# Optimization experiments

Hardware: AMD Instinct MI355X
Metric: run time of the kernel (lower is better)

## Reference

```python
import jax, jax.numpy as jnp
import numpy as np

B, S, D, H = 2, 2048, 1024, 16
HD = D // H  # head_dim = 64


def setup_inputs() -> dict:
    key = jax.random.key(0)
    ks = jax.random.split(key, 10)
    std = 1.0 / np.sqrt(D)
    inputs = jax.random.normal(ks[0], (B, S, D), dtype=jnp.float32)
    # stacked per-head projection weights: [H, HD, D] (row-major like nn.Linear)
    Wq = jax.random.uniform(ks[1], (H, HD, D), jnp.float32, -std, std)
    bq = jax.random.uniform(ks[2], (H, HD), jnp.float32, -std, std)
    Wk = jax.random.uniform(ks[3], (H, HD, D), jnp.float32, -std, std)
    bk = jax.random.uniform(ks[4], (H, HD), jnp.float32, -std, std)
    Wv = jax.random.uniform(ks[5], (H, HD, D), jnp.float32, -std, std)
    bv = jax.random.uniform(ks[6], (H, HD), jnp.float32, -std, std)
    Wo = jax.random.uniform(ks[7], (D, D), jnp.float32, -std, std)
    bo = jax.random.uniform(ks[8], (D,), jnp.float32, -std, std)
    return {"inputs": inputs, "Wq": Wq, "bq": bq, "Wk": Wk, "bk": bk,
            "Wv": Wv, "bv": bv, "Wo": Wo, "bo": bo}


def reference(inputs, Wq, bq, Wk, bk, Wv, bv, Wo, bo):
    # per-head projections, batched over heads: [B,H,S,HD]
    q = jnp.einsum('bsd,hed->bhse', inputs, Wq) + bq[None, :, None, :]
    k = jnp.einsum('bsd,hed->bhse', inputs, Wk) + bk[None, :, None, :]
    v = jnp.einsum('bsd,hed->bhse', inputs, Wv) + bv[None, :, None, :]
    scale = 1.0 / np.sqrt(HD).astype(np.float32)
    # explicit [B,H,S,S] score matrix, as in the original naive attention
    scores = jnp.einsum('bhqe,bhke->bhqk', q, k) * scale
    causal = jnp.tril(jnp.ones((S, S), dtype=bool))
    scores = jnp.where(causal[None, None], scores, jnp.float32(-jnp.inf))
    attn = jax.nn.softmax(scores, axis=-1)  # dropout p=0 -> identity
    wv = jnp.einsum('bhqk,bhke->bhqe', attn, v)
    # concat heads along feature dim: [B,S,H*HD] = [B,S,D]
    z = wv.transpose(0, 2, 1, 3).reshape(B, S, D)
    out = jnp.einsum('bsd,ed->bse', z, Wo) + bo
    return out
```

## Files before the change

### kernel.cpp

```cpp
#include <hip/hip_runtime.h>
#include <math.h>

#define Bx 2
#define Sx 2048
#define Dx 1024
#define Hx 16
#define HDx 64
#define Mx (Bx*Sx)

typedef __bf16 bf16x8 __attribute__((ext_vector_type(8)));
typedef __bf16 bf16x4 __attribute__((ext_vector_type(4)));
typedef float  f32x4  __attribute__((ext_vector_type(4)));

#define SCL 0.18033688011112042f

__device__ __forceinline__ void gload_lds16(const __bf16* g, __bf16* l) {
  __builtin_amdgcn_global_load_lds(
      (const __attribute__((address_space(1))) unsigned int*)g,
      (__attribute__((address_space(3))) unsigned int*)l, 16, 0, 0);
}

__device__ __forceinline__ void cvt8(const float* s, __bf16* d) {
  float4 a = *(const float4*)s;
  float4 b = *(const float4*)(s + 4);
  bf16x8 o;
  o[0] = (__bf16)a.x; o[1] = (__bf16)a.y; o[2] = (__bf16)a.z; o[3] = (__bf16)a.w;
  o[4] = (__bf16)b.x; o[5] = (__bf16)b.y; o[6] = (__bf16)b.z; o[7] = (__bf16)b.w;
  *(bf16x8*)d = o;
}

__global__ __launch_bounds__(256) void cvt_kernel(
    const float* __restrict__ x, const float* __restrict__ Wq,
    const float* __restrict__ Wk, const float* __restrict__ Wv,
    const float* __restrict__ Wo, const float* __restrict__ bq,
    const float* __restrict__ bk, const float* __restrict__ bv,
    __bf16* __restrict__ xb, __bf16* __restrict__ wqkv,
    __bf16* __restrict__ wob, float* __restrict__ bqkv)
{
  const int bid = blockIdx.x;
  const int t = threadIdx.x;
  const size_t MEG = 1024u * 1024u;
  if (bid < 2048) {
    size_t e = (size_t)bid * 2048 + t * 8;
    cvt8(x + e, xb + e);
  } else if (bid < 3584) {
    size_t e = (size_t)(bid - 2048) * 2048 + t * 8;
    const float* src = (e < MEG) ? (Wq + e) : (e < 2 * MEG) ? (Wk + (e - MEG)) : (Wv + (e - 2 * MEG));
    cvt8(src, wqkv + e);
  } else if (bid < 4096) {
    size_t e = (size_t)(bid - 3584) * 2048 + t * 8;
    cvt8(Wo + e, wob + e);
  } else {
    for (int i = t; i < 3072; i += 256)
      bqkv[i] = (i < 1024) ? bq[i] : (i < 2048) ? bk[i - 1024] : bv[i - 2048];
  }
}

template<int TM, int TN, int MODE>
__global__ __launch_bounds__(256) void gemm_k(
    const __bf16* __restrict__ A, const __bf16* __restrict__ W,
    const float* __restrict__ bias, float* __restrict__ Cf,
    __bf16* __restrict__ Cb, __bf16* __restrict__ vT,
    int M, int N, int K, int ldc)
{
  constexpr int MS = TM / 32;
  constexpr int NS = TN / 32;
  __shared__ __bf16 As[TM * 64];
  __shared__ __bf16 Bs[TN * 64];
  const int tid = threadIdx.x;
  const int lane = tid & 63, wave = tid >> 6;
  const int l16 = lane & 15, quad = lane >> 4;
  const int wm = (wave >> 1) * (TM / 2);
  const int wn = (wave & 1) * (TN / 2);
  const int m0 = blockIdx.y * TM;
  const int n0 = blockIdx.x * TN;
  const int swz = l16 & 7;

  const f32x4 zero = {0.f, 0.f, 0.f, 0.f};
  f32x4 acc[MS][NS];
#pragma unroll
  for (int i = 0; i < MS; ++i)
#pragma unroll
    for (int j = 0; j < NS; ++j) acc[i][j] = zero;

  const int srow = tid >> 3;
  const int scs = (tid & 7) ^ (srow & 7);
  const __bf16* Ag = A + (size_t)(m0 + srow) * K + scs * 8;
  const __bf16* Wg = W + (size_t)(n0 + srow) * K + scs * 8;

  for (int k0 = 0; k0 < K; k0 += 64) {
    __syncthreads();
#pragma unroll
    for (int i = 0; i < TM / 32; ++i)
      gload_lds16(Ag + (size_t)(i * 32) * K + k0, &As[(i * 256 + tid) * 8]);
#pragma unroll
    for (int i = 0; i < TN / 32; ++i)
      gload_lds16(Wg + (size_t)(i * 32) * K + k0, &Bs[(i * 256 + tid) * 8]);
    __syncthreads();

#pragma unroll
    for (int hk = 0; hk < 2; ++hk) {
      const int ph = ((hk * 4 + quad) ^ swz) * 8;
      bf16x8 af[MS], bfr[NS];
#pragma unroll
      for (int i = 0; i < MS; ++i)
        af[i] = *(const bf16x8*)&As[(wm + i * 16 + l16) * 64 + ph];
#pragma unroll
      for (int j = 0; j < NS; ++j)
        bfr[j] = *(const bf16x8*)&Bs[(wn + j * 16 + l16) * 64 + ph];
#pragma unroll
      for (int i = 0; i < MS; ++i)
#pragma unroll
        for (int j = 0; j < NS; ++j)
          acc[i][j] = __builtin_amdgcn_mfma_f32_16x16x32_bf16(af[i], bfr[j], acc[i][j], 0, 0, 0);
    }
  }

  const int cbase = n0 + wn + l16;
#pragma unroll
  for (int j = 0; j < NS; ++j) {
    const int c = cbase + j * 16;
    const float bv_ = bias[c];
#pragma unroll
    for (int i = 0; i < MS; ++i) {
      const int r0 = m0 + wm + i * 16 + quad * 4;
      if (MODE == 0) {
#pragma unroll
        for (int g = 0; g < 4; ++g)
          Cf[(size_t)(r0 + g) * ldc + c] = acc[i][j][g] + bv_;
      } else {
        if (c < 2048) {
          const float sc = (c < 1024) ? SCL : 1.0f;
#pragma unroll
          for (int g = 0; g < 4; ++g)
            Cb[(size_t)(r0 + g) * 3072 + c] = (__bf16)((acc[i][j][g] + bv_) * sc);
        } else {
          const int c2 = c - 2048;
          const int hh = c2 >> 6, dd = c2 & 63;
          const int bb = r0 >> 11, ss = r0 & 2047;
          bf16x4 st;
          st[0] = (__bf16)(acc[i][j][0] + bv_);
          st[1] = (__bf16)(acc[i][j][1] + bv_);
          st[2] = (__bf16)(acc[i][j][2] + bv_);
          st[3] = (__bf16)(acc[i][j][3] + bv_);
          *(bf16x4*)&vT[((size_t)(bb * 16 + hh) * 64 + dd) * 2048 + ss] = st;
        }
      }
    }
  }
}

__global__ __launch_bounds__(256) void attn_mfma(
    const __bf16* __restrict__ qkv, const __bf16* __restrict__ vT,
    __bf16* __restrict__ zb)
{
  __shared__ __bf16 Qs[64 * 64];
  __shared__ __bf16 Ks[2][64 * 64];
  __shared__ __bf16 Vs[3][64 * 64];

  const int tid = threadIdx.x;
  const int lane = tid & 63, wave = tid >> 6;
  const int l16 = lane & 15, quad = lane >> 4;
  const int bx = blockIdx.x;
  const int qt = 31 - (bx >> 5);
  const int bh = bx & 31;
  const int h = bh & 15, b = bh >> 4;
  const int q0 = qt * 64;

  const __bf16* qg = qkv + (size_t)b * 2048 * 3072 + h * 64;
  const __bf16* kg = qg + 1024;
  const __bf16* vg = vT + (size_t)bh * 64 * 2048;

#define STAGE_KV(kt_, kbuf, vbuf)                                               \
  { const int kn = (kt_) * 64;                                                  \
    _Pragma("unroll")                                                           \
    for (int i = 0; i < 2; ++i) {                                               \
      int slot = i * 256 + tid;                                                 \
      int row = slot >> 3, ph2 = slot & 7;                                      \
      int cs = ph2 ^ (row & 7);                                                 \
      gload_lds16(kg + (size_t)(kn + row) * 3072 + cs * 8, &Ks[kbuf][slot * 8]);\
      gload_lds16(vg + (size_t)row * 2048 + kn + cs * 8, &Vs[vbuf][slot * 8]);  \
    } }

#pragma unroll
  for (int i = 0; i < 2; ++i) {
    int slot = i * 256 + tid;
    int row = slot >> 3, ph2 = slot & 7;
    int cs = ph2 ^ (row & 7);
    gload_lds16(qg + (size_t)(q0 + row) * 3072 + cs * 8, &Qs[slot * 8]);
  }
  STAGE_KV(0, 0, 0)
  __syncthreads();

  const int sw0 = ((quad) ^ (l16 & 7)) * 8;
  const int sw1 = ((quad + 4) ^ (l16 & 7)) * 8;
  const int mrow = wave * 16 + l16;

  bf16x8 qf0 = *(const bf16x8*)&Qs[mrow * 64 + sw0];
  bf16x8 qf1 = *(const bf16x8*)&Qs[mrow * 64 + sw1];
  __bf16* P = &Qs[wave * 16 * 64];

  bf16x8 onesf;
  {
    __bf16 ov = (l16 == 0) ? (__bf16)1.0f : (__bf16)0.0f;
#pragma unroll
    for (int i = 0; i < 8; ++i) onesf[i] = ov;
  }

  const f32x4 zero = {0.f, 0.f, 0.f, 0.f};
  f32x4 O[4], Ol = zero;
#pragma unroll
  for (int j = 0; j < 4; ++j) O[j] = zero;
  f32x4 s_cur[4], s_next[4];

#define S_TILE(sdst, kb)                                                        \
  { _Pragma("unroll")                                                           \
    for (int j = 0; j < 4; ++j) sdst[j] = zero;                                 \
    _Pragma("unroll")                                                           \
    for (int j = 0; j < 4; ++j) {                                               \
      bf16x8 kf0 = *(const bf16x8*)&Ks[kb][(j * 16 + l16) * 64 + sw0];          \
      sdst[j] = __builtin_amdgcn_mfma_f32_16x16x32_bf16(qf0, kf0, sdst[j],0,0,0);\
      bf16x8 kf1 = *(const bf16x8*)&Ks[kb][(j * 16 + l16) * 64 + sw1];          \
      sdst[j] = __builtin_amdgcn_mfma_f32_16x16x32_bf16(qf1, kf1, sdst[j],0,0,0);\
    } }

#define EXP_P(s, DIAG)                                                          \
  { _Pragma("unroll")                                                           \
    for (int j = 0; j < 4; ++j) {                                               \
      _Pragma("unroll")                                                         \
      for (int g = 0; g < 4; ++g) {                                             \
        float p = __builtin_exp2f(s[j][g]);                                     \
        if (DIAG && (j * 16 + l16) > (wave * 16 + quad * 4 + g)) p = 0.f;       \
        s[j][g] = p;                                                            \
      }                                                                         \
    }                                                                           \
    _Pragma("unroll")                                                           \
    for (int j = 0; j < 4; ++j) {                                               \
      const int col = j * 16 + l16;                                             \
      const int ch = col >> 3, cin = col & 7;                                   \
      _Pragma("unroll")                                                         \
      for (int g = 0; g < 4; ++g) {                                             \
        const int row = quad * 4 + g;                                           \
        P[row * 64 + ((ch ^ (row & 7)) * 8) + cin] = (__bf16)s[j][g];           \
      }                                                                         \
    } }

#define PV_TILE(vb)                                                             \
  { bf16x8 pf0 = *(const bf16x8*)&P[l16 * 64 + sw0];                            \
    bf16x8 pf1 = *(const bf16x8*)&P[l16 * 64 + sw1];                            \
    _Pragma("unroll")                                                           \
    for (int j = 0; j < 4; ++j) {                                               \
      bf16x8 vf0 = *(const bf16x8*)&Vs[vb][(j * 16 + l16) * 64 + sw0];          \
      O[j] = __builtin_amdgcn_mfma_f32_16x16x32_bf16(pf0, vf0, O[j], 0, 0, 0);  \
      bf16x8 vf1 = *(const bf16x8*)&Vs[vb][(j * 16 + l16) * 64 + sw1];          \
      O[j] = __builtin_amdgcn_mfma_f32_16x16x32_bf16(pf1, vf1, O[j], 0, 0, 0);  \
    }                                                                           \
    Ol = __builtin_amdgcn_mfma_f32_16x16x32_bf16(pf0, onesf, Ol, 0, 0, 0);      \
    Ol = __builtin_amdgcn_mfma_f32_16x16x32_bf16(pf1, onesf, Ol, 0, 0, 0); }

  if (qt > 0) STAGE_KV(1, 1, 1)
  S_TILE(s_cur, 0)
  if (qt > 0) __syncthreads();

  for (int t = 0; t < qt; ++t) {
    EXP_P(s_cur, false)
    S_TILE(s_next, (t + 1) & 1)
    PV_TILE(t % 3)
    if (t + 2 <= qt) STAGE_KV(t + 2, t & 1, (t + 2) % 3)
    __syncthreads();
#pragma unroll
    for (int j = 0; j < 4; ++j) s_cur[j] = s_next[j];
  }
  EXP_P(s_cur, true)
  PV_TILE(qt % 3)

  const int rq = q0 + wave * 16 + quad * 4;
#pragma unroll
  for (int g = 0; g < 4; ++g) {
    const float lv = __shfl(Ol[g], quad * 16);
    const float inv = 1.0f / lv;
    const size_t rb = (size_t)(b * 2048 + rq + g) * 1024 + h * 64 + l16;
#pragma unroll
    for (int j = 0; j < 4; ++j)
      zb[rb + j * 16] = (__bf16)(O[j][g] * inv);
  }
}

extern "C" void kernel_launch(void* const* d_in, const int* in_sizes, int n_in,
                              void* d_out, int out_size, void* d_ws, size_t ws_size,
                              hipStream_t stream) {
  (void)in_sizes; (void)n_in; (void)out_size; (void)ws_size;
  const float* x  = (const float*)d_in[0];
  const float* Wq = (const float*)d_in[1];
  const float* bq = (const float*)d_in[2];
  const float* Wk = (const float*)d_in[3];
  const float* bk = (const float*)d_in[4];
  const float* Wv = (const float*)d_in[5];
  const float* bv = (const float*)d_in[6];
  const float* Wo = (const float*)d_in[7];
  const float* bo = (const float*)d_in[8];

  char* ws = (char*)d_ws;
  __bf16* xb   = (__bf16*)(ws);
  __bf16* wqkv = (__bf16*)(ws + (8ull  << 20));
  __bf16* wob  = (__bf16*)(ws + (14ull << 20));
  float*  bqkv = (float*) (ws + (16ull << 20));
  __bf16* qkv  = (__bf16*)(ws + (17ull << 20));
  __bf16* vT   = (__bf16*)(ws + (41ull << 20));
  __bf16* zb   = (__bf16*)(ws + (49ull << 20));

  cvt_kernel<<<4097, 256, 0, stream>>>(x, Wq, Wk, Wv, Wo, bq, bk, bv,
                                       xb, wqkv, wob, bqkv);
  gemm_k<128, 128, 1><<<dim3(24, 32), 256, 0, stream>>>(
      xb, wqkv, bqkv, nullptr, qkv, vT, Mx, 3072, 1024, 0);
  attn_mfma<<<1024, 256, 0, stream>>>(qkv, vT, zb);
  gemm_k<128, 64, 0><<<dim3(16, 32), 256, 0, stream>>>(
      zb, wob, bo, (float*)d_out, nullptr, nullptr, Mx, 1024, 1024, 1024);
}
```

Baseline: 196.3 us.

## Enlarge attention query tile to 128 rows with two sub-tiles per wave

The attention kernel now processes 128 query rows per block (32 per wave as two 16-row sub-tiles), so each K/V tile loaded into LDS feeds twice as many MFMAs and global K/V traffic per query is halved. K and V staging is split and both use double buffers, with loads issued at the top of each iteration. Blocks are ordered heavy-first then light to balance causal work, and the grid is halved to 512 blocks. The cost is more registers per thread, fewer blocks in flight and more work wasted on diagonal masking.

Result: slower. 212.1 us (+8.0%).

```diff
diff --git a/kernel.cpp b/kernel.cpp
--- a/kernel.cpp
+++ b/kernel.cpp
@@ -154,51 +154,65 @@
     const __bf16* __restrict__ qkv, const __bf16* __restrict__ vT,
     __bf16* __restrict__ zb)
 {
-  __shared__ __bf16 Qs[64 * 64];
+  __shared__ __bf16 Qs[128 * 64];
   __shared__ __bf16 Ks[2][64 * 64];
-  __shared__ __bf16 Vs[3][64 * 64];
+  __shared__ __bf16 Vs[2][64 * 64];
 
   const int tid = threadIdx.x;
   const int lane = tid & 63, wave = tid >> 6;
   const int l16 = lane & 15, quad = lane >> 4;
+  const int swz = l16 & 7;
   const int bx = blockIdx.x;
-  const int qt = 31 - (bx >> 5);
+  const int qtg = bx >> 5;
+  const int qt = (qtg < 8) ? (15 - qtg) : (qtg - 8);
   const int bh = bx & 31;
   const int h = bh & 15, b = bh >> 4;
-  const int q0 = qt * 64;
+  const int q0 = qt * 128;
+  const int nk = 2 * qt + 2;
 
   const __bf16* qg = qkv + (size_t)b * 2048 * 3072 + h * 64;
   const __bf16* kg = qg + 1024;
   const __bf16* vg = vT + (size_t)bh * 64 * 2048;
 
-#define STAGE_KV(kt_, kbuf, vbuf)                                               \
+#define STAGE_K(kt_, kb)                                                        \
   { const int kn = (kt_) * 64;                                                  \
     _Pragma("unroll")                                                           \
     for (int i = 0; i < 2; ++i) {                                               \
       int slot = i * 256 + tid;                                                 \
-      int row = slot >> 3, ph2 = slot & 7;                                      \
-      int cs = ph2 ^ (row & 7);                                                 \
-      gload_lds16(kg + (size_t)(kn + row) * 3072 + cs * 8, &Ks[kbuf][slot * 8]);\
-      gload_lds16(vg + (size_t)row * 2048 + kn + cs * 8, &Vs[vbuf][slot * 8]);  \
+      int row = slot >> 3;                                                      \
+      int cs = (slot & 7) ^ (row & 7);                                          \
+      gload_lds16(kg + (size_t)(kn + row) * 3072 + cs * 8, &Ks[kb][slot * 8]);  \
     } }
 
-#pragma unroll
-  for (int i = 0; i < 2; ++i) {
+#define STAGE_V(kt_, vb)                                                        \
+  { const int kn = (kt_) * 64;                                                  \
+    _Pragma("unroll")                                                           \
+    for (int i = 0; i < 2; ++i) {                                               \
+      int slot = i * 256 + tid;                                                 \
+      int row = slot >> 3;                                                      \
+      int cs = (slot & 7) ^ (row & 7);                                          \
+      gload_lds16(vg + (size_t)row * 2048 + kn + cs * 8, &Vs[vb][slot * 8]);    \
+    } }
+
+#pragma unroll
+  for (int i = 0; i < 4; ++i) {
     int slot = i * 256 + tid;
-    int row = slot >> 3, ph2 = slot & 7;
-    int cs = ph2 ^ (row & 7);
+    int row = slot >> 3;
+    int cs = (slot & 7) ^ (row & 7);
     gload_lds16(qg + (size_t)(q0 + row) * 3072 + cs * 8, &Qs[slot * 8]);
   }
-  STAGE_KV(0, 0, 0)
+  STAGE_K(0, 0)
+  STAGE_V(0, 0)
+  STAGE_K(1, 1)
   __syncthreads();
 
-  const int sw0 = ((quad) ^ (l16 & 7)) * 8;
-  const int sw1 = ((quad + 4) ^ (l16 & 7)) * 8;
-  const int mrow = wave * 16 + l16;
-
-  bf16x8 qf0 = *(const bf16x8*)&Qs[mrow * 64 + sw0];
-  bf16x8 qf1 = *(const bf16x8*)&Qs[mrow * 64 + sw1];
-  __bf16* P = &Qs[wave * 16 * 64];
+  bf16x8 qf[2][2];
+#pragma unroll
+  for (int s = 0; s < 2; ++s)
+#pragma unroll
+    for (int kk = 0; kk < 2; ++kk)
+      qf[s][kk] = *(const bf16x8*)&Qs[(wave * 32 + s * 16 + l16) * 64 + ((kk * 4 + quad) ^ swz) * 8];
+  __bf16* P = &Qs[wave * 32 * 64];
 
   bf16x8 onesf;
   {
@@ -208,81 +222,108 @@
   }
 
   const f32x4 zero = {0.f, 0.f, 0.f, 0.f};
-  f32x4 O[4], Ol = zero;
-#pragma unroll
-  for (int j = 0; j < 4; ++j) O[j] = zero;
-  f32x4 s_cur[4], s_next[4];
-
-#define S_TILE(sdst, kb)                                                        \
+  f32x4 O[2][4], Ol[2];
+#pragma unroll
+  for (int s = 0; s < 2; ++s) {
+    Ol[s] = zero;
+#pragma unroll
+    for (int j = 0; j < 4; ++j) O[s][j] = zero;
+  }
+  f32x4 s_cur[2][4], s_next[2][4];
+
+#define S_TILE(sd, kb)                                                          \
   { _Pragma("unroll")                                                           \
-    for (int j = 0; j < 4; ++j) sdst[j] = zero;                                 \
+    for (int s = 0; s < 2; ++s)                                                 \
+      _Pragma("unroll")                                                         \
+      for (int j = 0; j < 4; ++j) sd[s][j] = zero;                              \
     _Pragma("unroll")                                                           \
-    for (int j = 0; j < 4; ++j) {                                               \
-      bf16x8 kf0 = *(const bf16x8*)&Ks[kb][(j * 16 + l16) * 64 + sw0];          \
-      sdst[j] = __builtin_amdgcn_mfma_f32_16x16x32_bf16(qf0, kf0, sdst[j],0,0,0);\
-      bf16x8 kf1 = *(const bf16x8*)&Ks[kb][(j * 16 + l16) * 64 + sw1];          \
-      sdst[j] = __builtin_amdgcn_mfma_f32_16x16x32_bf16(qf1, kf1, sdst[j],0,0,0);\
+    for (int kk = 0; kk < 2; ++kk)                                              \
+      _Pragma("unroll")                                                         \
+      for (int j = 0; j < 4; ++j) {                                             \
+        bf16x8 kf = *(const bf16x8*)&Ks[kb][(j * 16 + l16) * 64 + ((kk * 4 + quad) ^ swz) * 8]; \
+        sd[0][j] = __builtin_amdgcn_mfma_f32_16x16x32_bf16(qf[0][kk], kf, sd[0][j], 0, 0, 0);  \
+        sd[1][j] = __builtin_amdgcn_mfma_f32_16x16x32_bf16(qf[1][kk], kf, sd[1][j], 0, 0, 0);  \
+      } }
+
+#define EXP_P(sv, MASK, k0_)                                                    \
+  { _Pragma("unroll")                                                           \
+    for (int s = 0; s < 2; ++s)                                                 \
+      _Pragma("unroll")                                                         \
+      for (int j = 0; j < 4; ++j) {                                             \
+        const int cg = (k0_) + j * 16 + l16;                                    \
+        _Pragma("unroll")                                                       \
+        for (int g = 0; g < 4; ++g) {                                           \
+          float p = __builtin_exp2f(sv[s][j][g]);                               \
+          if (MASK && cg > (q0 + wave * 32 + s * 16 + quad * 4 + g)) p = 0.f;   \
+          sv[s][j][g] = p;                                                      \
+        }                                                                       \
+      }                                                                         \
+    _Pragma("unroll")                                                           \
+    for (int s = 0; s < 2; ++s)                                                 \
+      _Pragma("unroll")                                                         \
+      for (int j = 0; j < 4; ++j) {                                             \
+        const int ch = j * 2 + (l16 >> 3);                                      \
+        _Pragma("unroll")                                                       \
+        for (int g = 0; g < 4; ++g) {                                           \
+          const int rl = s * 16 + quad * 4 + g;                                 \
+          P[rl * 64 + ((ch ^ (rl & 7)) * 8) + (l16 & 7)] = (__bf16)sv[s][j][g]; \
+        }                                                                       \
+      } }
+
+#define PV_TILE(vb)                                                             \
+  { _Pragma("unroll")                                                           \
+    for (int kk = 0; kk < 2; ++kk) {                                            \
+      bf16x8 pf0 = *(const bf16x8*)&P[(l16) * 64 + ((kk * 4 + quad) ^ swz) * 8];         \
+      bf16x8 pf1 = *(const bf16x8*)&P[(16 + l16) * 64 + ((kk * 4 + quad) ^ swz) * 8];    \
+      _Pragma("unroll")                                                         \
+      for (int j = 0; j < 4; ++j) {                                             \
+        bf16x8 vf = *(const bf16x8*)&Vs[vb][(j * 16 + l16) * 64 + ((kk * 4 + quad) ^ swz) * 8]; \
+        O[0][j] = __builtin_amdgcn_mfma_f32_16x16x32_bf16(pf0, vf, O[0][j], 0, 0, 0);    \
+        O[1][j] = __builtin_amdgcn_mfma_f32_16x16x32_bf16(pf1, vf, O[1][j], 0, 0, 0);    \
+      }                                                                         \
+      Ol[0] = __builtin_amdgcn_mfma_f32_16x16x32_bf16(pf0, onesf, Ol[0], 0, 0, 0);       \
+      Ol[1] = __builtin_amdgcn_mfma_f32_16x16x32_bf16(pf1, onesf, Ol[1], 0, 0, 0);       \
     } }
 
-#define EXP_P(s, DIAG)                                                          \
+#define SCOPY                                                                   \
   { _Pragma("unroll")                                                           \
-    for (int j = 0; j < 4; ++j) {                                               \
-      _Pragma("unroll")                                                         \
-      for (int g = 0; g < 4; ++g) {                                             \
-        float p = __builtin_exp2f(s[j][g]);                                     \
-        if (DIAG && (j * 16 + l16) > (wave * 16 + quad * 4 + g)) p = 0.f;       \
-        s[j][g] = p;                                                            \
-      }                                                                         \
-    }                                                                           \
-    _Pragma("unroll")                                                           \
-    for (int j = 0; j < 4; ++j) {                                               \
-      const int col = j * 16 + l16;                                             \
-      const int ch = col >> 3, cin = col & 7;                                   \
-      _Pragma("unroll")                                                         \
-      for (int g = 0; g < 4; ++g) {                                             \
-        const int row = quad * 4 + g;                                           \
-        P[row * 64 + ((ch ^ (row & 7)) * 8) + cin] = (__bf16)s[j][g];           \
-      }                                                                         \
-    } }
-
-#define PV_TILE(vb)                                                             \
-  { bf16x8 pf0 = *(const bf16x8*)&P[l16 * 64 + sw0];                            \
-    bf16x8 pf1 = *(const bf16x8*)&P[l16 * 64 + sw1];                            \
-    _Pragma("unroll")                                                           \
-    for (int j = 0; j < 4; ++j) {                                               \
-      bf16x8 vf0 = *(const bf16x8*)&Vs[vb][(j * 16 + l16) * 64 + sw0];          \
-      O[j] = __builtin_amdgcn_mfma_f32_16x16x32_bf16(pf0, vf0, O[j], 0, 0, 0);  \
-      bf16x8 vf1 = *(const bf16x8*)&Vs[vb][(j * 16 + l16) * 64 + sw1];          \
-      O[j] = __builtin_amdgcn_mfma_f32_16x16x32_bf16(pf1, vf1, O[j], 0, 0, 0);  \
-    }                                                                           \
-    Ol = __builtin_amdgcn_mfma_f32_16x16x32_bf16(pf0, onesf, Ol, 0, 0, 0);      \
-    Ol = __builtin_amdgcn_mfma_f32_16x16x32_bf16(pf1, onesf, Ol, 0, 0, 0); }
-
-  if (qt > 0) STAGE_KV(1, 1, 1)
+    for (int s = 0; s < 2; ++s)                                                 \
+      _Pragma("unroll")                                                         \
+      for (int j = 0; j < 4; ++j) s_cur[s][j] = s_next[s][j]; }
+
   S_TILE(s_cur, 0)
-  if (qt > 0) __syncthreads();
-
-  for (int t = 0; t < qt; ++t) {
-    EXP_P(s_cur, false)
+  __syncthreads();
+
+  for (int t = 0; t <= nk - 3; ++t) {
+    STAGE_K(t + 2, t & 1)
+    STAGE_V(t + 1, (t + 1) & 1)
+    EXP_P(s_cur, false, t * 64)
     S_TILE(s_next, (t + 1) & 1)
-    PV_TILE(t % 3)
-    if (t + 2 <= qt) STAGE_KV(t + 2, t & 1, (t + 2) % 3)
+    PV_TILE(t & 1)
     __syncthreads();
-#pragma unroll
-    for (int j = 0; j < 4; ++j) s_cur[j] = s_next[j];
-  }
-  EXP_P(s_cur, true)
-  PV_TILE(qt % 3)
-
-  const int rq = q0 + wave * 16 + quad * 4;
-#pragma unroll
-  for (int g = 0; g < 4; ++g) {
-    const float lv = __shfl(Ol[g], quad * 16);
-    const float inv = 1.0f / lv;
-    const size_t rb = (size_t)(b * 2048 + rq + g) * 1024 + h * 64 + l16;
-#pragma unroll
-    for (int j = 0; j < 4; ++j)
-      zb[rb + j * 16] = (__bf16)(O[j][g] * inv);
+    SCOPY
+  }
+  STAGE_V(nk - 1, (nk - 1) & 1)
+  EXP_P(s_cur, true, (nk - 2) * 64)
+  S_TILE(s_next, (nk - 1) & 1)
+  PV_TILE((nk - 2) & 1)
+  __syncthreads();
+  SCOPY
+  EXP_P(s_cur, true, (nk - 1) * 64)
+  PV_TILE((nk - 1) & 1)
+
+#pragma unroll
+  for (int s = 0; s < 2; ++s) {
+#pragma unroll
+    for (int g = 0; g < 4; ++g) {
+      const float lv = __shfl(Ol[s][g], quad * 16);
+      const float inv = 1.0f / lv;
+      const int rq = q0 + wave * 32 + s * 16 + quad * 4 + g;
+      const size_t rb = (size_t)(b * 2048 + rq) * 1024 + h * 64 + l16;
+#pragma unroll
+      for (int j = 0; j < 4; ++j)
+        zb[rb + j * 16] = (__bf16)(O[s][j][g] * inv);
+    }
   }
 }
 
@@ -313,7 +354,7 @@
                                        xb, wqkv, wob, bqkv);
   gemm_k<128, 128, 1><<<dim3(24, 32), 256, 0, stream>>>(
       xb, wqkv, bqkv, nullptr, qkv, vT, Mx, 3072, 1024, 0);
-  attn_mfma<<<1024, 256, 0, stream>>>(qkv, vT, zb);
+  attn_mfma<<<512, 256, 0, stream>>>(qkv, vT, zb);
   gemm_k<128, 64, 0><<<dim3(16, 32), 256, 0, stream>>>(
       zb, wob, bo, (float*)d_out, nullptr, nullptr, Mx, 1024, 1024, 1024);
 }
```
